# Optimization experiments

Hardware: AMD Instinct MI355X
Metric: run time of the kernel (lower is better)

The kernel has to match this reference:

```python
import jax, jax.numpy as jnp
import numpy as np

T, H, F, E, K = 4096, 1024, 2048, 8, 2

def setup_inputs() -> dict:
    key = jax.random.key(0)
    k1, k2, k3, k4, k5, k6 = jax.random.split(key, 6)
    scale = 1.0 / np.sqrt(H)
    return {
        "x": jax.random.normal(k1, (T, H), dtype=jnp.float32),
        "expert_ids": jax.random.randint(k2, (T, K), 0, E, dtype=jnp.int32),
        "expert_weights": jax.random.uniform(k3, (T, K), dtype=jnp.float32),
        "gate_weights": jax.random.normal(k4, (E, H, F), dtype=jnp.float32) * scale,
        "up_weights": jax.random.normal(k5, (E, H, F), dtype=jnp.float32) * scale,
        "down_weights": jax.random.normal(k6, (E, F, H), dtype=jnp.float32) * scale,
    }


def reference(x, expert_ids, expert_weights, gate_weights, up_weights, down_weights):
    # Faithful MoE dispatch/combine. The torch module sorts assignments by
    # expert, runs gate/up/down GEMMs per expert on the gathered tokens, and
    # scatter-adds weight * expert_out back per (token, slot) assignment.
    # Equivalent math: for each expert e, each token accumulates
    # (sum of its routing weights for slots routed to e) * FFN_e(x_token).
    num_experts = gate_weights.shape[0]
    out = jnp.zeros_like(x)
    for e in range(num_experts):
        # coeff[t] = sum_k expert_weights[t,k] * (expert_ids[t,k] == e)
        coeff = jnp.sum(jnp.where(expert_ids == e, expert_weights, 0.0), axis=1)  # [T]
        g = x @ gate_weights[e]           # [T, F]
        u = x @ up_weights[e]             # [T, F]
        y = (jax.nn.silu(g) * u) @ down_weights[e]  # [T, H]
        out = out + coeff[:, None] * y
    return out
```

## Files before the change

### kernel.cpp

```cpp
#include <hip/hip_runtime.h>
#include <hip/hip_bf16.h>

#define Td 4096
#define Hd 1024
#define Fd 2048
#define Ed 8

#define BM 128
#define BN 128
#define BK 32
#define LDA 40

typedef short bf16x8 __attribute__((ext_vector_type(8)));
typedef float f32x4 __attribute__((ext_vector_type(4)));

__device__ __forceinline__ unsigned short f2bf(float f) {
  union { float f; unsigned u; } v; v.f = f;
  unsigned r = v.u + 0x7FFFu + ((v.u >> 16) & 1u);
  return (unsigned short)(r >> 16);
}

__global__ void prep_transpose_kernel(const float* __restrict__ gw,
                                      const float* __restrict__ uw,
                                      const float* __restrict__ dw,
                                      unsigned short* __restrict__ gt,
                                      unsigned short* __restrict__ ut,
                                      unsigned short* __restrict__ dt) {
  const int m = blockIdx.z % 3;
  const int e = blockIdx.z / 3;
  const int R = (m == 2) ? Fd : Hd;
  const int C = (m == 2) ? Hd : Fd;
  const int r0 = blockIdx.y * 64, c0 = blockIdx.x * 64;
  if (r0 >= R || c0 >= C) return;
  const float* src = ((m == 0) ? gw : (m == 1) ? uw : dw) + (size_t)e * Hd * Fd;
  unsigned short* dst = ((m == 0) ? gt : (m == 1) ? ut : dt) + (size_t)e * Hd * Fd;
  __shared__ unsigned short tile[64][68];
  const int tr = threadIdx.x >> 4;
  const int tc = (threadIdx.x & 15) * 4;
#pragma unroll
  for (int i = 0; i < 4; ++i) {
    const int r = tr + i * 16;
    const float4 v = *(const float4*)(src + (size_t)(r0 + r) * C + c0 + tc);
    tile[r][tc + 0] = f2bf(v.x);
    tile[r][tc + 1] = f2bf(v.y);
    tile[r][tc + 2] = f2bf(v.z);
    tile[r][tc + 3] = f2bf(v.w);
  }
  __syncthreads();
#pragma unroll
  for (int i = 0; i < 4; ++i) {
    const int c = tr + i * 16;
    ushort4 o;
    o.x = tile[tc + 0][c];
    o.y = tile[tc + 1][c];
    o.z = tile[tc + 2][c];
    o.w = tile[tc + 3][c];
    *(ushort4*)(dst + (size_t)(c0 + c) * R + r0 + tc) = o;
  }
}

__global__ void routing_kernel(const int* __restrict__ ids,
                               const float* __restrict__ w,
                               int* __restrict__ cnt, int* __restrict__ base,
                               int* __restrict__ tok, float* __restrict__ cof) {
  __shared__ int lcnt[Ed], lbase[Ed], lpos[Ed];
  const int t = threadIdx.x;
  if (t < Ed) { lcnt[t] = 0; lpos[t] = 0; }
  __syncthreads();
  for (int i = t; i < Td; i += blockDim.x) {
    const int e0 = ids[i * 2], e1 = ids[i * 2 + 1];
    atomicAdd(&lcnt[e0], 1);
    if (e1 != e0) atomicAdd(&lcnt[e1], 1);
  }
  __syncthreads();
  if (t == 0) {
    int s = 0;
    for (int e = 0; e < Ed; ++e) { lbase[e] = s; s += lcnt[e]; }
  }
  __syncthreads();
  for (int i = t; i < Td; i += blockDim.x) {
    const int e0 = ids[i * 2], e1 = ids[i * 2 + 1];
    const float w0 = w[i * 2], w1 = w[i * 2 + 1];
    if (e0 == e1) {
      const int p = atomicAdd(&lpos[e0], 1);
      tok[lbase[e0] + p] = i; cof[lbase[e0] + p] = w0 + w1;
    } else {
      int p = atomicAdd(&lpos[e0], 1);
      tok[lbase[e0] + p] = i; cof[lbase[e0] + p] = w0;
      p = atomicAdd(&lpos[e1], 1);
      tok[lbase[e1] + p] = i; cof[lbase[e1] + p] = w1;
    }
  }
  __syncthreads();
  if (t < Ed) { cnt[t] = lcnt[t]; base[t] = lbase[t]; }
}

__global__ __launch_bounds__(256)
void gateup_kernel(const float* __restrict__ x,
                   const unsigned short* __restrict__ gate_t,
                   const unsigned short* __restrict__ up_t,
                   const int* __restrict__ cnt, const int* __restrict__ base,
                   const int* __restrict__ tok, const float* __restrict__ cof,
                   unsigned short* __restrict__ act) {
  const int e = blockIdx.z, mt = blockIdx.y, nt = blockIdx.x;
  const int cn = cnt[e];
  if (mt * BM >= cn) return;
  const int b0 = base[e];

  __shared__ unsigned short A_lds[BM][LDA];
  __shared__ unsigned short Bg_lds[BN][LDA];
  __shared__ unsigned short Bu_lds[BN][LDA];
  __shared__ int tok_l[BM];
  __shared__ float cof_l[BM];

  const int tid = threadIdx.x;
  if (tid < BM) {
    const int r = mt * BM + tid;
    tok_l[tid] = (r < cn) ? tok[b0 + r] : 0;
    cof_l[tid] = (r < cn) ? cof[b0 + r] : 0.f;
  }

  const unsigned short* gp = gate_t + (size_t)e * Fd * Hd + (size_t)(nt * BN) * Hd;
  const unsigned short* upw = up_t  + (size_t)e * Fd * Hd + (size_t)(nt * BN) * Hd;

  const int lane = tid & 63;
  const int wave = tid >> 6;
  const int wm = wave >> 1;
  const int wn = wave & 1;
  const int fr16 = lane & 15;
  const int k8 = (lane >> 4) * 8;

  f32x4 accg[4][4], accu[4][4];
#pragma unroll
  for (int i = 0; i < 4; ++i)
#pragma unroll
    for (int j = 0; j < 4; ++j) {
      accg[i][j] = (f32x4){0.f, 0.f, 0.f, 0.f};
      accu[i][j] = (f32x4){0.f, 0.f, 0.f, 0.f};
    }

  const int sr = tid >> 1;
  const int sk = (tid & 1) * 16;
  const bool rvalid = (mt * BM + sr) < cn;

  __syncthreads();
  const size_t xoff = (size_t)tok_l[sr] * Hd + sk;

  for (int k0 = 0; k0 < Hd; k0 += BK) {
    __syncthreads();
    {
      bf16x8 t0 = 0, t1 = 0;
      if (rvalid) {
        const float* xp = x + xoff + k0;
        const float4 v0 = *(const float4*)(xp + 0);
        const float4 v1 = *(const float4*)(xp + 4);
        const float4 v2 = *(const float4*)(xp + 8);
        const float4 v3 = *(const float4*)(xp + 12);
        t0[0] = (short)f2bf(v0.x); t0[1] = (short)f2bf(v0.y);
        t0[2] = (short)f2bf(v0.z); t0[3] = (short)f2bf(v0.w);
        t0[4] = (short)f2bf(v1.x); t0[5] = (short)f2bf(v1.y);
        t0[6] = (short)f2bf(v1.z); t0[7] = (short)f2bf(v1.w);
        t1[0] = (short)f2bf(v2.x); t1[1] = (short)f2bf(v2.y);
        t1[2] = (short)f2bf(v2.z); t1[3] = (short)f2bf(v2.w);
        t1[4] = (short)f2bf(v3.x); t1[5] = (short)f2bf(v3.y);
        t1[6] = (short)f2bf(v3.z); t1[7] = (short)f2bf(v3.w);
      }
      *(bf16x8*)&A_lds[sr][sk + 0] = t0;
      *(bf16x8*)&A_lds[sr][sk + 8] = t1;
    }
    {
      const unsigned short* g1 = gp  + (size_t)sr * Hd + k0 + sk;
      const unsigned short* u1 = upw + (size_t)sr * Hd + k0 + sk;
      *(uint4*)&Bg_lds[sr][sk + 0] = *(const uint4*)(g1 + 0);
      *(uint4*)&Bg_lds[sr][sk + 8] = *(const uint4*)(g1 + 8);
      *(uint4*)&Bu_lds[sr][sk + 0] = *(const uint4*)(u1 + 0);
      *(uint4*)&Bu_lds[sr][sk + 8] = *(const uint4*)(u1 + 8);
    }
    __syncthreads();

    bf16x8 af[4], bg[4], bu[4];
#pragma unroll
    for (int f = 0; f < 4; ++f)
      af[f] = *(const bf16x8*)&A_lds[wm * 64 + f * 16 + fr16][k8];
#pragma unroll
    for (int f = 0; f < 4; ++f) {
      bg[f] = *(const bf16x8*)&Bg_lds[wn * 64 + f * 16 + fr16][k8];
      bu[f] = *(const bf16x8*)&Bu_lds[wn * 64 + f * 16 + fr16][k8];
    }
#pragma unroll
    for (int fm = 0; fm < 4; ++fm)
#pragma unroll
      for (int fn = 0; fn < 4; ++fn) {
        accg[fm][fn] = __builtin_amdgcn_mfma_f32_16x16x32_bf16(af[fm], bg[fn], accg[fm][fn], 0, 0, 0);
        accu[fm][fn] = __builtin_amdgcn_mfma_f32_16x16x32_bf16(af[fm], bu[fn], accu[fm][fn], 0, 0, 0);
      }
  }

  const int row4 = (lane >> 4) * 4;
#pragma unroll
  for (int fm = 0; fm < 4; ++fm) {
#pragma unroll
    for (int fn = 0; fn < 4; ++fn) {
#pragma unroll
      for (int r = 0; r < 4; ++r) {
        const int rr = wm * 64 + fm * 16 + row4 + r;
        const int grow = mt * BM + rr;
        if (grow < cn) {
          const float g = accg[fm][fn][r];
          const float u = accu[fm][fn][r];
          const float a = (g / (1.f + __expf(-g))) * u * cof_l[rr];
          const int col = nt * BN + wn * 64 + fn * 16 + fr16;
          act[(size_t)(b0 + grow) * Fd + col] = f2bf(a);
        }
      }
    }
  }
}

__global__ __launch_bounds__(256)
void down_kernel(const unsigned short* __restrict__ act,
                 const unsigned short* __restrict__ down_t,
                 const int* __restrict__ cnt, const int* __restrict__ base,
                 const int* __restrict__ tok,
                 float* __restrict__ out) {
  const int e = blockIdx.z, mt = blockIdx.y, nt = blockIdx.x;
  const int cn = cnt[e];
  if (mt * BM >= cn) return;
  const int b0 = base[e];

  __shared__ unsigned short A_lds[BM][LDA];
  __shared__ unsigned short B_lds[BN][LDA];
  __shared__ int tok_l[BM];

  const int tid = threadIdx.x;
  if (tid < BM) {
    const int r = mt * BM + tid;
    tok_l[tid] = (r < cn) ? tok[b0 + r] : 0;
  }

  const unsigned short* dp = down_t + (size_t)e * Hd * Fd + (size_t)(nt * BN) * Fd;

  const int lane = tid & 63;
  const int wave = tid >> 6;
  const int wm = wave >> 1;
  const int wn = wave & 1;
  const int fr16 = lane & 15;
  const int k8 = (lane >> 4) * 8;

  f32x4 acc[4][4];
#pragma unroll
  for (int i = 0; i < 4; ++i)
#pragma unroll
    for (int j = 0; j < 4; ++j) acc[i][j] = (f32x4){0.f, 0.f, 0.f, 0.f};

  const int sr = tid >> 1;
  const int sk = (tid & 1) * 16;
  const bool rvalid = (mt * BM + sr) < cn;
  const size_t arow = (size_t)(b0 + mt * BM + sr) * Fd + sk;

  for (int k0 = 0; k0 < Fd; k0 += BK) {
    __syncthreads();
    {
      bf16x8 t0 = 0, t1 = 0;
      if (rvalid) {
        const unsigned short* ap = act + arow + k0;
        t0 = *(const bf16x8*)(ap + 0);
        t1 = *(const bf16x8*)(ap + 8);
      }
      *(bf16x8*)&A_lds[sr][sk + 0] = t0;
      *(bf16x8*)&A_lds[sr][sk + 8] = t1;
      const unsigned short* bp = dp + (size_t)sr * Fd + k0 + sk;
      *(uint4*)&B_lds[sr][sk + 0] = *(const uint4*)(bp + 0);
      *(uint4*)&B_lds[sr][sk + 8] = *(const uint4*)(bp + 8);
    }
    __syncthreads();

    bf16x8 af[4], bf[4];
#pragma unroll
    for (int f = 0; f < 4; ++f) {
      af[f] = *(const bf16x8*)&A_lds[wm * 64 + f * 16 + fr16][k8];
      bf[f] = *(const bf16x8*)&B_lds[wn * 64 + f * 16 + fr16][k8];
    }
#pragma unroll
    for (int fm = 0; fm < 4; ++fm)
#pragma unroll
      for (int fn = 0; fn < 4; ++fn)
        acc[fm][fn] = __builtin_amdgcn_mfma_f32_16x16x32_bf16(af[fm], bf[fn], acc[fm][fn], 0, 0, 0);
  }

  const int row4 = (lane >> 4) * 4;
#pragma unroll
  for (int fm = 0; fm < 4; ++fm) {
#pragma unroll
    for (int fn = 0; fn < 4; ++fn) {
#pragma unroll
      for (int r = 0; r < 4; ++r) {
        const int rr = wm * 64 + fm * 16 + row4 + r;
        if (mt * BM + rr < cn) {
          const int col = nt * BN + wn * 64 + fn * 16 + fr16;
          atomicAdd(&out[(size_t)tok_l[rr] * Hd + col], acc[fm][fn][r]);
        }
      }
    }
  }
}

extern "C" void kernel_launch(void* const* d_in, const int* in_sizes, int n_in,
                              void* d_out, int out_size, void* d_ws, size_t ws_size,
                              hipStream_t stream) {
  const float* x  = (const float*)d_in[0];
  const int*   ids = (const int*)d_in[1];
  const float* w  = (const float*)d_in[2];
  const float* gw = (const float*)d_in[3];
  const float* uw = (const float*)d_in[4];
  const float* dw = (const float*)d_in[5];
  float* out = (float*)d_out;

  const size_t SZW = (size_t)Ed * Hd * Fd * 2;
  char* ws = (char*)d_ws;
  unsigned short* gt  = (unsigned short*)(ws);
  unsigned short* ut  = (unsigned short*)(ws + SZW);
  unsigned short* dt  = (unsigned short*)(ws + 2 * SZW);
  unsigned short* act = (unsigned short*)(ws + 3 * SZW);
  char* meta = ws + 3 * SZW + (size_t)8192 * Fd * 2;
  int*   cnt  = (int*)meta;
  int*   base = (int*)(meta + 32);
  int*   tok  = (int*)(meta + 64);
  float* cof  = (float*)(meta + 64 + 8192 * 4);

  hipMemsetAsync(d_out, 0, (size_t)Td * Hd * 4, stream);
  prep_transpose_kernel<<<dim3(32, 32, 24), 256, 0, stream>>>(gw, uw, dw, gt, ut, dt);
  routing_kernel<<<1, 1024, 0, stream>>>(ids, w, cnt, base, tok, cof);
  gateup_kernel<<<dim3(Fd / BN, Td / BM, Ed), 256, 0, stream>>>(x, gt, ut, cnt, base, tok, cof, act);
  down_kernel<<<dim3(Hd / BN, Td / BM, Ed), 256, 0, stream>>>(act, dt, cnt, base, tok, out);
}
```

Measured before the change: 514.8 us.

## Use direct global-to-LDS loads with XOR swizzle, BK=64, pre-converted bf16 x, ballot routing

Converts x to bf16 once in a separate kernel so the gate/up GEMM no longer converts fp32 to bf16 inside its K loop. Both GEMM kernels now fill shared memory with global_load_lds 16-byte direct loads into an XOR-swizzled unpadded layout, and the K tile doubles to 64. Routing replaces per-thread LDS atomics with wave ballots and popcount prefix offsets. The down kernel clamps out-of-range activation rows instead of zero-filling them, relying on masked stores, and the launcher now returns silently if the workspace is too small.

```diff
diff --git a/kernel.cpp b/kernel.cpp
--- a/kernel.cpp
+++ b/kernel.cpp
@@ -5,11 +5,9 @@
 #define Hd 1024
 #define Fd 2048
 #define Ed 8
-
 #define BM 128
 #define BN 128
-#define BK 32
-#define LDA 40
+#define BK 64
 
 typedef short bf16x8 __attribute__((ext_vector_type(8)));
 typedef float f32x4 __attribute__((ext_vector_type(4)));
@@ -18,6 +16,25 @@
   union { float f; unsigned u; } v; v.f = f;
   unsigned r = v.u + 0x7FFFu + ((v.u >> 16) & 1u);
   return (unsigned short)(r >> 16);
+}
+
+__device__ __forceinline__ void gload16(const unsigned short* g, unsigned short* l) {
+  __builtin_amdgcn_global_load_lds(
+      (const __attribute__((address_space(1))) unsigned int*)g,
+      (__attribute__((address_space(3))) unsigned int*)l,
+      16, 0, 0);
+}
+
+__global__ void xconv_kernel(const float* __restrict__ x, unsigned short* __restrict__ xb) {
+  const int i = (blockIdx.x * 256 + threadIdx.x) * 8;
+  const float4 v0 = *(const float4*)(x + i);
+  const float4 v1 = *(const float4*)(x + i + 4);
+  bf16x8 o;
+  o[0] = (short)f2bf(v0.x); o[1] = (short)f2bf(v0.y);
+  o[2] = (short)f2bf(v0.z); o[3] = (short)f2bf(v0.w);
+  o[4] = (short)f2bf(v1.x); o[5] = (short)f2bf(v1.y);
+  o[6] = (short)f2bf(v1.z); o[7] = (short)f2bf(v1.w);
+  *(bf16x8*)(xb + i) = o;
 }
 
 __global__ void prep_transpose_kernel(const float* __restrict__ gw,
@@ -65,12 +82,19 @@
                                int* __restrict__ tok, float* __restrict__ cof) {
   __shared__ int lcnt[Ed], lbase[Ed], lpos[Ed];
   const int t = threadIdx.x;
+  const int lane = t & 63;
   if (t < Ed) { lcnt[t] = 0; lpos[t] = 0; }
   __syncthreads();
-  for (int i = t; i < Td; i += blockDim.x) {
-    const int e0 = ids[i * 2], e1 = ids[i * 2 + 1];
-    atomicAdd(&lcnt[e0], 1);
-    if (e1 != e0) atomicAdd(&lcnt[e1], 1);
+  for (int i = t; i < Td; i += 1024) {
+    const int e0 = ids[2 * i], e1 = ids[2 * i + 1];
+    const int em = (e1 == e0) ? -1 : e1;
+#pragma unroll
+    for (int e = 0; e < Ed; ++e) {
+      unsigned long long m0 = __ballot(e0 == e);
+      unsigned long long m1 = __ballot(em == e);
+      int n = __popcll(m0) + __popcll(m1);
+      if (lane == 0 && n) atomicAdd(&lcnt[e], n);
+    }
   }
   __syncthreads();
   if (t == 0) {
@@ -78,17 +102,29 @@
     for (int e = 0; e < Ed; ++e) { lbase[e] = s; s += lcnt[e]; }
   }
   __syncthreads();
-  for (int i = t; i < Td; i += blockDim.x) {
-    const int e0 = ids[i * 2], e1 = ids[i * 2 + 1];
-    const float w0 = w[i * 2], w1 = w[i * 2 + 1];
-    if (e0 == e1) {
-      const int p = atomicAdd(&lpos[e0], 1);
-      tok[lbase[e0] + p] = i; cof[lbase[e0] + p] = w0 + w1;
-    } else {
-      int p = atomicAdd(&lpos[e0], 1);
-      tok[lbase[e0] + p] = i; cof[lbase[e0] + p] = w0;
-      p = atomicAdd(&lpos[e1], 1);
-      tok[lbase[e1] + p] = i; cof[lbase[e1] + p] = w1;
+  const unsigned long long below = (1ull << lane) - 1ull;
+  for (int i = t; i < Td; i += 1024) {
+    const int e0 = ids[2 * i], e1 = ids[2 * i + 1];
+    const float w0 = w[2 * i], w1 = w[2 * i + 1];
+    const bool mg = (e1 == e0);
+    const int em = mg ? -1 : e1;
+#pragma unroll
+    for (int e = 0; e < Ed; ++e) {
+      unsigned long long m0 = __ballot(e0 == e);
+      unsigned long long m1 = __ballot(em == e);
+      const int n0 = __popcll(m0);
+      const int n = n0 + __popcll(m1);
+      int p = 0;
+      if (lane == 0 && n) p = atomicAdd(&lpos[e], n);
+      p = __shfl(p, 0);
+      if (e0 == e) {
+        const int r = lbase[e] + p + __popcll(m0 & below);
+        tok[r] = i; cof[r] = mg ? (w0 + w1) : w0;
+      }
+      if (em == e) {
+        const int r = lbase[e] + p + n0 + __popcll(m1 & below);
+        tok[r] = i; cof[r] = w1;
+      }
     }
   }
   __syncthreads();
@@ -96,9 +132,8 @@
 }
 
 __global__ __launch_bounds__(256)
-void gateup_kernel(const float* __restrict__ x,
+void gateup_kernel(const unsigned short* __restrict__ xb,
                    const unsigned short* __restrict__ gate_t,
-                   const unsigned short* __restrict__ up_t,
                    const int* __restrict__ cnt, const int* __restrict__ base,
                    const int* __restrict__ tok, const float* __restrict__ cof,
                    unsigned short* __restrict__ act) {
@@ -107,9 +142,9 @@
   if (mt * BM >= cn) return;
   const int b0 = base[e];
 
-  __shared__ unsigned short A_lds[BM][LDA];
-  __shared__ unsigned short Bg_lds[BN][LDA];
-  __shared__ unsigned short Bu_lds[BN][LDA];
+  __shared__ unsigned short A_lds[BM * BK];
+  __shared__ unsigned short Bg_lds[BN * BK];
+  __shared__ unsigned short Bu_lds[BN * BK];
   __shared__ int tok_l[BM];
   __shared__ float cof_l[BM];
 
@@ -119,16 +154,26 @@
     tok_l[tid] = (r < cn) ? tok[b0 + r] : 0;
     cof_l[tid] = (r < cn) ? cof[b0 + r] : 0.f;
   }
-
-  const unsigned short* gp = gate_t + (size_t)e * Fd * Hd + (size_t)(nt * BN) * Hd;
-  const unsigned short* upw = up_t  + (size_t)e * Fd * Hd + (size_t)(nt * BN) * Hd;
+  __syncthreads();
 
   const int lane = tid & 63;
   const int wave = tid >> 6;
-  const int wm = wave >> 1;
-  const int wn = wave & 1;
+  const int wm = wave >> 1, wn = wave & 1;
   const int fr16 = lane & 15;
-  const int k8 = (lane >> 4) * 8;
+  const int jb = lane >> 4;
+  const int rx7 = lane & 7;
+
+  const int sw = ((lane & 7) ^ (lane >> 3)) * 8;
+  const unsigned short* gwp = gate_t + (size_t)e * Fd * Hd;
+  const unsigned short* ap[4];
+  const unsigned short* gp[4];
+#pragma unroll
+  for (int i = 0; i < 4; ++i) {
+    const int rl = wave * 32 + i * 8 + (lane >> 3);
+    ap[i] = xb + (size_t)tok_l[rl] * Hd + sw;
+    gp[i] = gwp + (size_t)(nt * BN + rl) * Hd + sw;
+  }
+  const size_t UPOFF = (size_t)Ed * Fd * Hd;
 
   f32x4 accg[4][4], accu[4][4];
 #pragma unroll
@@ -139,61 +184,35 @@
       accu[i][j] = (f32x4){0.f, 0.f, 0.f, 0.f};
     }
 
-  const int sr = tid >> 1;
-  const int sk = (tid & 1) * 16;
-  const bool rvalid = (mt * BM + sr) < cn;
-
-  __syncthreads();
-  const size_t xoff = (size_t)tok_l[sr] * Hd + sk;
-
   for (int k0 = 0; k0 < Hd; k0 += BK) {
     __syncthreads();
-    {
-      bf16x8 t0 = 0, t1 = 0;
-      if (rvalid) {
-        const float* xp = x + xoff + k0;
-        const float4 v0 = *(const float4*)(xp + 0);
-        const float4 v1 = *(const float4*)(xp + 4);
-        const float4 v2 = *(const float4*)(xp + 8);
-        const float4 v3 = *(const float4*)(xp + 12);
-        t0[0] = (short)f2bf(v0.x); t0[1] = (short)f2bf(v0.y);
-        t0[2] = (short)f2bf(v0.z); t0[3] = (short)f2bf(v0.w);
-        t0[4] = (short)f2bf(v1.x); t0[5] = (short)f2bf(v1.y);
-        t0[6] = (short)f2bf(v1.z); t0[7] = (short)f2bf(v1.w);
-        t1[0] = (short)f2bf(v2.x); t1[1] = (short)f2bf(v2.y);
-        t1[2] = (short)f2bf(v2.z); t1[3] = (short)f2bf(v2.w);
-        t1[4] = (short)f2bf(v3.x); t1[5] = (short)f2bf(v3.y);
-        t1[6] = (short)f2bf(v3.z); t1[7] = (short)f2bf(v3.w);
-      }
-      *(bf16x8*)&A_lds[sr][sk + 0] = t0;
-      *(bf16x8*)&A_lds[sr][sk + 8] = t1;
-    }
-    {
-      const unsigned short* g1 = gp  + (size_t)sr * Hd + k0 + sk;
-      const unsigned short* u1 = upw + (size_t)sr * Hd + k0 + sk;
-      *(uint4*)&Bg_lds[sr][sk + 0] = *(const uint4*)(g1 + 0);
-      *(uint4*)&Bg_lds[sr][sk + 8] = *(const uint4*)(g1 + 8);
-      *(uint4*)&Bu_lds[sr][sk + 0] = *(const uint4*)(u1 + 0);
-      *(uint4*)&Bu_lds[sr][sk + 8] = *(const uint4*)(u1 + 8);
+#pragma unroll
+    for (int i = 0; i < 4; ++i) {
+      gload16(ap[i] + k0,         A_lds  + wave * 2048 + i * 512);
+      gload16(gp[i] + k0,         Bg_lds + wave * 2048 + i * 512);
+      gload16(gp[i] + UPOFF + k0, Bu_lds + wave * 2048 + i * 512);
     }
     __syncthreads();
-
-    bf16x8 af[4], bg[4], bu[4];
-#pragma unroll
-    for (int f = 0; f < 4; ++f)
-      af[f] = *(const bf16x8*)&A_lds[wm * 64 + f * 16 + fr16][k8];
-#pragma unroll
-    for (int f = 0; f < 4; ++f) {
-      bg[f] = *(const bf16x8*)&Bg_lds[wn * 64 + f * 16 + fr16][k8];
-      bu[f] = *(const bf16x8*)&Bu_lds[wn * 64 + f * 16 + fr16][k8];
-    }
-#pragma unroll
-    for (int fm = 0; fm < 4; ++fm)
-#pragma unroll
-      for (int fn = 0; fn < 4; ++fn) {
-        accg[fm][fn] = __builtin_amdgcn_mfma_f32_16x16x32_bf16(af[fm], bg[fn], accg[fm][fn], 0, 0, 0);
-        accu[fm][fn] = __builtin_amdgcn_mfma_f32_16x16x32_bf16(af[fm], bu[fn], accu[fm][fn], 0, 0, 0);
-      }
+#pragma unroll
+    for (int kk = 0; kk < 2; ++kk) {
+      bf16x8 af[4], bg[4], bu[4];
+      const int slot = kk * 4 + jb;
+#pragma unroll
+      for (int f = 0; f < 4; ++f) {
+        const int ra = wm * 64 + f * 16 + fr16;
+        const int rb = wn * 64 + f * 16 + fr16;
+        af[f] = *(const bf16x8*)&A_lds [64 * ra + 8 * (slot ^ rx7)];
+        bg[f] = *(const bf16x8*)&Bg_lds[64 * rb + 8 * (slot ^ rx7)];
+        bu[f] = *(const bf16x8*)&Bu_lds[64 * rb + 8 * (slot ^ rx7)];
+      }
+#pragma unroll
+      for (int fm = 0; fm < 4; ++fm)
+#pragma unroll
+        for (int fn = 0; fn < 4; ++fn) {
+          accg[fm][fn] = __builtin_amdgcn_mfma_f32_16x16x32_bf16(af[fm], bg[fn], accg[fm][fn], 0, 0, 0);
+          accu[fm][fn] = __builtin_amdgcn_mfma_f32_16x16x32_bf16(af[fm], bu[fn], accu[fm][fn], 0, 0, 0);
+        }
+    }
   }
 
   const int row4 = (lane >> 4) * 4;
@@ -228,8 +247,8 @@
   if (mt * BM >= cn) return;
   const int b0 = base[e];
 
-  __shared__ unsigned short A_lds[BM][LDA];
-  __shared__ unsigned short B_lds[BN][LDA];
+  __shared__ unsigned short A_lds[BM * BK];
+  __shared__ unsigned short B_lds[BN * BK];
   __shared__ int tok_l[BM];
 
   const int tid = threadIdx.x;
@@ -238,54 +257,57 @@
     tok_l[tid] = (r < cn) ? tok[b0 + r] : 0;
   }
 
-  const unsigned short* dp = down_t + (size_t)e * Hd * Fd + (size_t)(nt * BN) * Fd;
-
   const int lane = tid & 63;
   const int wave = tid >> 6;
-  const int wm = wave >> 1;
-  const int wn = wave & 1;
+  const int wm = wave >> 1, wn = wave & 1;
   const int fr16 = lane & 15;
-  const int k8 = (lane >> 4) * 8;
+  const int jb = lane >> 4;
+  const int rx7 = lane & 7;
+
+  const int sw = ((lane & 7) ^ (lane >> 3)) * 8;
+  const unsigned short* dwp = down_t + (size_t)e * Hd * Fd;
+  const unsigned short* ap[4];
+  const unsigned short* bp[4];
+#pragma unroll
+  for (int i = 0; i < 4; ++i) {
+    const int rl = wave * 32 + i * 8 + (lane >> 3);
+    int rowg = b0 + mt * BM + rl;
+    if (rowg > 8191) rowg = 8191;
+    ap[i] = act + (size_t)rowg * Fd + sw;
+    bp[i] = dwp + (size_t)(nt * BN + rl) * Fd + sw;
+  }
 
   f32x4 acc[4][4];
 #pragma unroll
   for (int i = 0; i < 4; ++i)
 #pragma unroll
     for (int j = 0; j < 4; ++j) acc[i][j] = (f32x4){0.f, 0.f, 0.f, 0.f};
-
-  const int sr = tid >> 1;
-  const int sk = (tid & 1) * 16;
-  const bool rvalid = (mt * BM + sr) < cn;
-  const size_t arow = (size_t)(b0 + mt * BM + sr) * Fd + sk;
 
   for (int k0 = 0; k0 < Fd; k0 += BK) {
     __syncthreads();
-    {
-      bf16x8 t0 = 0, t1 = 0;
-      if (rvalid) {
-        const unsigned short* ap = act + arow + k0;
-        t0 = *(const bf16x8*)(ap + 0);
-        t1 = *(const bf16x8*)(ap + 8);
-      }
-      *(bf16x8*)&A_lds[sr][sk + 0] = t0;
-      *(bf16x8*)&A_lds[sr][sk + 8] = t1;
-      const unsigned short* bp = dp + (size_t)sr * Fd + k0 + sk;
-      *(uint4*)&B_lds[sr][sk + 0] = *(const uint4*)(bp + 0);
-      *(uint4*)&B_lds[sr][sk + 8] = *(const uint4*)(bp + 8);
+#pragma unroll
+    for (int i = 0; i < 4; ++i) {
+      gload16(ap[i] + k0, A_lds + wave * 2048 + i * 512);
+      gload16(bp[i] + k0, B_lds + wave * 2048 + i * 512);
     }
     __syncthreads();
-
-    bf16x8 af[4], bf[4];
-#pragma unroll
-    for (int f = 0; f < 4; ++f) {
-      af[f] = *(const bf16x8*)&A_lds[wm * 64 + f * 16 + fr16][k8];
-      bf[f] = *(const bf16x8*)&B_lds[wn * 64 + f * 16 + fr16][k8];
-    }
-#pragma unroll
-    for (int fm = 0; fm < 4; ++fm)
-#pragma unroll
-      for (int fn = 0; fn < 4; ++fn)
-        acc[fm][fn] = __builtin_amdgcn_mfma_f32_16x16x32_bf16(af[fm], bf[fn], acc[fm][fn], 0, 0, 0);
+#pragma unroll
+    for (int kk = 0; kk < 2; ++kk) {
+      bf16x8 af[4], bf[4];
+      const int slot = kk * 4 + jb;
+#pragma unroll
+      for (int f = 0; f < 4; ++f) {
+        const int ra = wm * 64 + f * 16 + fr16;
+        const int rb = wn * 64 + f * 16 + fr16;
+        af[f] = *(const bf16x8*)&A_lds[64 * ra + 8 * (slot ^ rx7)];
+        bf[f] = *(const bf16x8*)&B_lds[64 * rb + 8 * (slot ^ rx7)];
+      }
+#pragma unroll
+      for (int fm = 0; fm < 4; ++fm)
+#pragma unroll
+        for (int fn = 0; fn < 4; ++fn)
+          acc[fm][fn] = __builtin_amdgcn_mfma_f32_16x16x32_bf16(af[fm], bf[fn], acc[fm][fn], 0, 0, 0);
+    }
   }
 
   const int row4 = (lane >> 4) * 4;
@@ -317,20 +339,27 @@
   float* out = (float*)d_out;
 
   const size_t SZW = (size_t)Ed * Hd * Fd * 2;
+  const size_t ACT = (size_t)8192 * Fd * 2;
+  const size_t XB  = (size_t)Td * Hd * 2;
+  const size_t NEED = 3 * SZW + ACT + XB + 1 * 1024 * 1024;
+  if (ws_size < NEED) return;
+
   char* ws = (char*)d_ws;
-  unsigned short* gt  = (unsigned short*)(ws);
-  unsigned short* ut  = (unsigned short*)(ws + SZW);
-  unsigned short* dt  = (unsigned short*)(ws + 2 * SZW);
-  unsigned short* act = (unsigned short*)(ws + 3 * SZW);
-  char* meta = ws + 3 * SZW + (size_t)8192 * Fd * 2;
+  unsigned short* gt   = (unsigned short*)(ws);
+  unsigned short* ut   = (unsigned short*)(ws + SZW);
+  unsigned short* dt   = (unsigned short*)(ws + 2 * SZW);
+  unsigned short* act  = (unsigned short*)(ws + 3 * SZW);
+  unsigned short* xbuf = (unsigned short*)(ws + 3 * SZW + ACT);
+  char* meta = ws + 3 * SZW + ACT + XB;
   int*   cnt  = (int*)meta;
   int*   base = (int*)(meta + 32);
   int*   tok  = (int*)(meta + 64);
   float* cof  = (float*)(meta + 64 + 8192 * 4);
 
   hipMemsetAsync(d_out, 0, (size_t)Td * Hd * 4, stream);
+  xconv_kernel<<<Td * Hd / 8 / 256, 256, 0, stream>>>(x, xbuf);
+  routing_kernel<<<1, 1024, 0, stream>>>(ids, w, cnt, base, tok, cof);
   prep_transpose_kernel<<<dim3(32, 32, 24), 256, 0, stream>>>(gw, uw, dw, gt, ut, dt);
-  routing_kernel<<<1, 1024, 0, stream>>>(ids, w, cnt, base, tok, cof);
-  gateup_kernel<<<dim3(Fd / BN, Td / BM, Ed), 256, 0, stream>>>(x, gt, ut, cnt, base, tok, cof, act);
+  gateup_kernel<<<dim3(Fd / BN, Td / BM, Ed), 256, 0, stream>>>(xbuf, gt, cnt, base, tok, cof, act);
   down_kernel<<<dim3(Hd / BN, Td / BM, Ed), 256, 0, stream>>>(act, dt, cnt, base, tok, out);
 }
```

Result: faster. 439.6 us (-14.6%).
